# Kernel optimization log

Measured on AMD Instinct MI355X. Metric: run time of the kernel, lower is better.

## Reference

```python
import jax, jax.numpy as jnp
import numpy as np

HEADS = 8
DIM_HEAD = 64
DIM = 512
HIDDEN = HEADS * DIM_HEAD  # 512


def setup_inputs() -> dict:
    key = jax.random.key(0)
    k1, k2, k3, k4 = jax.random.split(key, 4)
    b, m, n = 4, 8, 512
    x = jax.random.normal(k1, (b, m, n, DIM), dtype=jnp.float32)
    pos_bias = jax.random.normal(k2, (HEADS, n, 16, 16), dtype=jnp.float32)
    # torch nn.Linear(dim, 3*hidden) weight is [3*hidden, dim]; we store the
    # transposed matmul form [dim, 3*hidden] for y = x @ W.
    w_qkv = jax.random.normal(k3, (DIM, 3 * HIDDEN), dtype=jnp.float32) * (DIM ** -0.5)
    w_out = jax.random.normal(k4, (HIDDEN, DIM), dtype=jnp.float32) * (HIDDEN ** -0.5)
    return {"x": x, "pos_bias": pos_bias, "w_qkv": w_qkv, "w_out": w_out}


def reference(x, pos_bias, w_qkv, w_out):
    b, m, n, _ = x.shape
    h, d = HEADS, DIM_HEAD
    scale = d ** -0.5
    qkv = jnp.einsum('bmnc,ce->bmne', x, w_qkv)  # [b,m,n,3*hidden]
    q, k, v = jnp.split(qkv, 3, axis=-1)
    # 'b m n (h d) -> (b m) h n d'
    def to_heads(t):
        return t.reshape(b * m, n, h, d).transpose(0, 2, 1, 3)
    q, k, v = to_heads(q), to_heads(k), to_heads(v)
    q = q * scale
    sim = jnp.einsum('bhid,bhjd->bhij', q, k)  # [(b*m), h, n, n]
    # pos_bias [h, n, p, q] -> mean over last two dims -> [h, n] -> broadcast [1,h,n,1]
    pb = pos_bias.mean(axis=(-2, -1))[None, :, :, None]
    sim = sim + pb
    sim = sim - jax.lax.stop_gradient(jnp.max(sim, axis=-1, keepdims=True))
    attn = jax.nn.softmax(sim, axis=-1)
    out = jnp.einsum('bhij,bhjd->bhid', attn, v)  # [(b*m), h, n, d]
    # '(b m) h n d -> b m n (h d)'
    out = out.transpose(0, 2, 1, 3).reshape(b, m, n, h * d)
    return jnp.einsum('bmne,ec->bmnc', out, w_out)
```

## Files before the change

kernel.cpp:

```cpp
#include <hip/hip_runtime.h>
#include <stdint.h>


typedef __attribute__((ext_vector_type(8))) short bf16x8;
typedef __attribute__((ext_vector_type(4))) float f32x4;
typedef __attribute__((ext_vector_type(4))) unsigned short us4;
typedef __attribute__((ext_vector_type(4))) float float4v;

__device__ __forceinline__ unsigned short f2b(float f) {
  union { float f; uint32_t u; } x; x.f = f;
  uint32_t r = x.u + 0x7fffu + ((x.u >> 16) & 1u);
  return (unsigned short)(r >> 16);
}

__device__ __forceinline__ uint32_t cvtpk(float lo, float hi) {
  uint32_t r;
  asm("v_cvt_pk_bf16_f32 %0, %1, %2" : "=v"(r) : "v"(lo), "v"(hi));
  return r;
}

__device__ __forceinline__ f32x4 mfma16(bf16x8 a, bf16x8 b, f32x4 c) {
  return __builtin_amdgcn_mfma_f32_16x16x32_bf16(a, b, c, 0, 0, 0);
}

__device__ __forceinline__ void gload_lds16(const unsigned short* g, unsigned short* l) {
  __builtin_amdgcn_global_load_lds(
      (const __attribute__((address_space(1))) unsigned int*)g,
      (__attribute__((address_space(3))) unsigned int*)l, 16, 0, 0);
}

__global__ __launch_bounds__(256) void prep_kernel(
    const float* __restrict__ x, unsigned short* __restrict__ xb,
    const float* __restrict__ wq, unsigned short* __restrict__ wqbT,
    const float* __restrict__ wo, unsigned short* __restrict__ wobT) {
  const int bid = blockIdx.x;
  if (bid < 8192) {
    size_t i = ((size_t)bid * 256 + threadIdx.x) * 4;
    float4v v = *(const float4v*)(x + i);
    us4 o;
#pragma unroll
    for (int j = 0; j < 4; ++j) o[j] = f2b(v[j]);
    *(us4*)(xb + i) = o;
    return;
  }
  __shared__ float tile[64][65];
  const float* src;
  unsigned short* dst;
  int R, C, bx, by;
  float scl = 1.0f;
  if (bid < 8192 + 192) {
    int q = bid - 8192;
    src = wq; dst = wqbT; R = 512; C = 1536; bx = q % 24; by = q / 24;
    if (bx * 64 < 512) scl = 0.125f;
  } else {
    int q = bid - 8384;
    src = wo; dst = wobT; R = 512; C = 512; bx = q % 8; by = q / 8;
  }
  const int tc0 = bx * 64, tr0 = by * 64;
#pragma unroll
  for (int k2 = 0; k2 < 16; ++k2) {
    int idx = threadIdx.x + k2 * 256;
    int r = idx >> 6, c = idx & 63;
    tile[r][c] = src[(size_t)(tr0 + r) * C + tc0 + c];
  }
  __syncthreads();
#pragma unroll
  for (int k2 = 0; k2 < 16; ++k2) {
    int idx = threadIdx.x + k2 * 256;
    int c = idx >> 6, r = idx & 63;
    dst[(size_t)(tc0 + c) * R + tr0 + r] = f2b(tile[r][c] * scl);
  }
}

__device__ __forceinline__ void gemm_core(
    const unsigned short* __restrict__ A, const unsigned short* __restrict__ Bt,
    int r0, int c0, unsigned short* As, unsigned short* Bs,
    f32x4 (&acc)[4][4]) {
  const int tid = threadIdx.x;
  const int lane = tid & 63;
  const int wave = tid >> 6;
  const int wr = (wave >> 1) * 64;
  const int wc = (wave & 1) * 64;
  const int l15 = lane & 15;
  const int g = lane >> 4;
  const int lsw = l15 & 7;

#pragma unroll
  for (int m = 0; m < 4; ++m)
#pragma unroll
    for (int n = 0; n < 4; ++n) acc[m][n] = (f32x4){0.f, 0.f, 0.f, 0.f};

  auto stage = [&](int kt, int b) {
#pragma unroll
    for (int i = 0; i < 4; ++i) {
      int chunk = tid + i * 256;
      int row = chunk >> 3;
      int csw = (chunk & 7) ^ (row & 7);
      gload_lds16(A + (size_t)(r0 + row) * 512 + kt + csw * 8,
                  As + b * 8192 + chunk * 8);
      gload_lds16(Bt + (size_t)(c0 + row) * 512 + kt + csw * 8,
                  Bs + b * 8192 + chunk * 8);
    }
  };

  stage(0, 0);
  asm volatile("s_waitcnt vmcnt(0)" ::: "memory");
  __builtin_amdgcn_s_barrier();

  int cur = 0;
#pragma unroll
  for (int t = 0; t < 8; ++t) {
    if (t < 7) stage((t + 1) * 64, cur ^ 1);
    const unsigned short* as = As + cur * 8192;
    const unsigned short* bs = Bs + cur * 8192;
#pragma unroll
    for (int ks = 0; ks < 2; ++ks) {
      bf16x8 af[4], bfr[4];
      const int cj = ((g + ks * 4) ^ lsw) * 8;
#pragma unroll
      for (int m = 0; m < 4; ++m)
        af[m] = *(const bf16x8*)(as + (wr + m * 16 + l15) * 64 + cj);
#pragma unroll
      for (int n = 0; n < 4; ++n)
        bfr[n] = *(const bf16x8*)(bs + (wc + n * 16 + l15) * 64 + cj);
      __builtin_amdgcn_s_setprio(1);
#pragma unroll
      for (int m = 0; m < 4; ++m)
#pragma unroll
        for (int n = 0; n < 4; ++n) acc[m][n] = mfma16(af[m], bfr[n], acc[m][n]);
      __builtin_amdgcn_s_setprio(0);
    }
    if (t < 7) {
      asm volatile("s_waitcnt vmcnt(0)" ::: "memory");
      __builtin_amdgcn_s_barrier();
      cur ^= 1;
    }
  }
  __syncthreads();
}

__global__ __launch_bounds__(256) void gemm_qkv_kernel(
    const unsigned short* __restrict__ xb, const unsigned short* __restrict__ wqbT,
    unsigned short* __restrict__ qb, unsigned short* __restrict__ kb,
    unsigned short* __restrict__ vtb) {
  __shared__ unsigned short smem[32768];
  f32x4 acc[4][4];
  const int bid = blockIdx.x;
  const int wgid = (bid & 7) * 192 + (bid >> 3);
  const int r0 = (wgid / 12) * 128;
  const int c0 = (wgid % 12) * 128;
  gemm_core(xb, wqbT, r0, c0, smem, smem + 16384, acc);

  const int tid = threadIdx.x, lane = tid & 63, wave = tid >> 6;
  const int wr = (wave >> 1) * 64, wc = (wave & 1) * 64;
  const int l15 = lane & 15, g = lane >> 4;
  const int part = c0 >> 9;

  if (part < 2) {
#pragma unroll
    for (int m = 0; m < 4; ++m) {
      int rbase = wr + m * 16 + 4 * g;
#pragma unroll
      for (int n = 0; n < 4; ++n) {
        int c = wc + n * 16 + l15;
        int c2 = c >> 3, ci = c & 7;
#pragma unroll
        for (int rr = 0; rr < 4; ++rr) {
          int r = rbase + rr;
          smem[r * 128 + ((c2 ^ (r & 15)) << 3) + ci] = f2b(acc[m][n][rr]);
        }
      }
    }
    __syncthreads();
    unsigned short* dstb = (part == 0) ? qb : kb;
#pragma unroll
    for (int it = 0; it < 8; ++it) {
      int idx = tid + it * 256;
      int r = idx >> 4, c2 = idx & 15;
      bf16x8 v = *(const bf16x8*)(smem + r * 128 + ((c2 ^ (r & 15)) << 3));
      int e = c0 + c2 * 8;
      int rem = e & 511, h = rem >> 6, d = rem & 63;
      int ig = r0 + r;
      int bh = (ig >> 9) * 8 + h, i = ig & 511;
      *(bf16x8*)(dstb + ((size_t)bh * 512 + i) * 64 + d) = v;
    }
  } else {
#pragma unroll
    for (int m = 0; m < 4; ++m) {
      int rbase = wr + m * 16 + 4 * g;
      int r2 = rbase >> 3, rhalf = rbase & 7;
#pragma unroll
      for (int n = 0; n < 4; ++n) {
        int c = wc + n * 16 + l15;
        us4 v;
#pragma unroll
        for (int rr = 0; rr < 4; ++rr) v[rr] = f2b(acc[m][n][rr]);
        *(us4*)(smem + c * 128 + ((r2 ^ (c & 15)) << 3) + rhalf) = v;
      }
    }
    __syncthreads();
#pragma unroll
    for (int it = 0; it < 8; ++it) {
      int idx = tid + it * 256;
      int c = idx >> 4, r8 = idx & 15;
      bf16x8 v = *(const bf16x8*)(smem + c * 128 + ((r8 ^ (c & 15)) << 3));
      int e = c0 + c;
      int rem = e & 511, h = rem >> 6, d = rem & 63;
      int ig0 = r0 + r8 * 8;
      int bh = (ig0 >> 9) * 8 + h, i = ig0 & 511;
      *(bf16x8*)(vtb + ((size_t)bh * 64 + d) * 512 + i) = v;
    }
  }
}

__global__ __launch_bounds__(256) void gemm_out_kernel(
    const unsigned short* __restrict__ ao, const unsigned short* __restrict__ wobT,
    float* __restrict__ out) {
  __shared__ unsigned short smem[32768];
  f32x4 acc[4][4];
  const int bid = blockIdx.x;
  const int wgid = (bid & 7) * 64 + (bid >> 3);
  const int r0 = (wgid >> 2) * 128;
  const int c0 = (wgid & 3) * 128;
  gemm_core(ao, wobT, r0, c0, smem, smem + 16384, acc);

  const int tid = threadIdx.x, lane = tid & 63, wave = tid >> 6;
  const int wr = (wave >> 1) * 64, wc = (wave & 1) * 64;
  const int l15 = lane & 15, g = lane >> 4;
#pragma unroll
  for (int m = 0; m < 4; ++m) {
    int i0g = r0 + wr + m * 16 + 4 * g;
#pragma unroll
    for (int n = 0; n < 4; ++n) {
      int e = c0 + wc + n * 16 + l15;
#pragma unroll
      for (int rr = 0; rr < 4; ++rr)
        out[(size_t)(i0g + rr) * 512 + e] = acc[m][n][rr];
    }
  }
}

__global__ __launch_bounds__(512, 4) void attn_kernel(
    const unsigned short* __restrict__ qb, const unsigned short* __restrict__ kb,
    const unsigned short* __restrict__ vtb, unsigned short* __restrict__ ao) {
  __shared__ unsigned short kbuf[2][8192];
  __shared__ unsigned short vbuf[2][8192];
  __shared__ unsigned short Ps[8][16][40];
  const int bh = blockIdx.x;
  const int qt = blockIdx.y;
  const int tid = threadIdx.x, lane = tid & 63, wave = tid >> 6;
  const int l15 = lane & 15, g = lane >> 4;
  const int qrow0 = qt * 128 + wave * 16;

  const unsigned short* Q = qb + ((size_t)bh * 512 + qrow0) * 64;
  const unsigned short* Kp = kb + (size_t)bh * 512 * 64;
  const unsigned short* Vt = vtb + (size_t)bh * 64 * 512;

  bf16x8 qf0 = *(const bf16x8*)(Q + l15 * 64 + g * 8);
  bf16x8 qf1 = *(const bf16x8*)(Q + l15 * 64 + 32 + g * 8);

  const int krow = tid >> 3;
  const int kck = (tid & 7) ^ (krow & 7);
  const int vrow = tid >> 4;
  const int vck = (tid & 15) ^ (vrow & 15);

  auto stage = [&](int t, int b) {
    const unsigned short* ks = Kp + ((size_t)t * 128 + krow) * 64 + kck * 8;
    gload_lds16(ks, kbuf[b] + tid * 8);
    gload_lds16(ks + 64 * 64, kbuf[b] + tid * 8 + 4096);
    const unsigned short* vs = Vt + (size_t)vrow * 512 + t * 128 + vck * 8;
    gload_lds16(vs, vbuf[b] + tid * 8);
    gload_lds16(vs + 32 * 512, vbuf[b] + tid * 8 + 4096);
  };

  f32x4 oacc[4];
#pragma unroll
  for (int m = 0; m < 4; ++m) oacc[m] = (f32x4){0.f, 0.f, 0.f, 0.f};
  float srow[4] = {0.f, 0.f, 0.f, 0.f};

  stage(0, 0);
  asm volatile("s_waitcnt vmcnt(0)" ::: "memory");
  __builtin_amdgcn_s_barrier();

  int cur = 0;
#pragma unroll
  for (int t = 0; t < 4; ++t) {
    if (t < 3) stage(t + 1, cur ^ 1);

    const unsigned short* kb_ = kbuf[cur];
    f32x4 s[8];
    const int c0i = g ^ (l15 & 7);
    __builtin_amdgcn_s_setprio(1);
#pragma unroll
    for (int tt = 0; tt < 8; ++tt) {
      int row = tt * 16 + l15;
      bf16x8 b0 = *(const bf16x8*)(kb_ + (row * 8 + c0i) * 8);
      bf16x8 b1 = *(const bf16x8*)(kb_ + (row * 8 + (c0i ^ 4)) * 8);
      f32x4 c = (f32x4){0.f, 0.f, 0.f, 0.f};
      c = mfma16(qf0, b0, c);
      s[tt] = mfma16(qf1, b1, c);
    }
    __builtin_amdgcn_s_setprio(0);

#pragma unroll
    for (int tt = 0; tt < 8; ++tt)
#pragma unroll
      for (int rr = 0; rr < 4; ++rr) {
        float e = __expf(s[tt][rr]);
        s[tt][rr] = e;
        srow[rr] += e;
      }

    const unsigned short* vb_ = vbuf[cur];
#pragma unroll
    for (int cc = 0; cc < 4; ++cc) {
#pragma unroll
      for (int rr = 0; rr < 4; ++rr) {
        uint32_t pk = cvtpk(s[cc * 2][rr], s[cc * 2 + 1][rr]);
        Ps[wave][4 * g + rr][l15] = (unsigned short)pk;
        Ps[wave][4 * g + rr][16 + l15] = (unsigned short)(pk >> 16);
      }
      asm volatile("s_waitcnt lgkmcnt(0)" ::: "memory");
      bf16x8 pf = *(const bf16x8*)(&Ps[wave][l15][g * 8]);
      __builtin_amdgcn_s_setprio(1);
#pragma unroll
      for (int m = 0; m < 4; ++m) {
        int vr = m * 16 + l15;
        bf16x8 vf = *(const bf16x8*)(vb_ + (vr * 16 + ((cc * 4 + g) ^ l15)) * 8);
        oacc[m] = mfma16(vf, pf, oacc[m]);
      }
      __builtin_amdgcn_s_setprio(0);
    }

    if (t < 3) {
      asm volatile("s_waitcnt vmcnt(0)" ::: "memory");
      __builtin_amdgcn_s_barrier();
      cur ^= 1;
    }
  }

#pragma unroll
  for (int rr = 0; rr < 4; ++rr)
#pragma unroll
    for (int o = 1; o < 16; o <<= 1) srow[rr] += __shfl_xor(srow[rr], o);
  int srcl = (l15 >> 2) * 16;
  float t0 = __shfl(srow[0], srcl), t1 = __shfl(srow[1], srcl);
  float t2 = __shfl(srow[2], srcl), t3 = __shfl(srow[3], srcl);
  int rq = l15 & 3;
  float sq = rq == 0 ? t0 : rq == 1 ? t1 : rq == 2 ? t2 : t3;
  float invq = 1.0f / sq;

  const int hh = bh & 7, bm = bh >> 3;
  unsigned short* aorow = ao + ((size_t)bm * 512 + qrow0 + l15) * 512 + hh * 64;
#pragma unroll
  for (int m = 0; m < 4; ++m) {
    union { us4 u; uint32_t w[2]; } uv;
    uv.w[0] = cvtpk(oacc[m][0] * invq, oacc[m][1] * invq);
    uv.w[1] = cvtpk(oacc[m][2] * invq, oacc[m][3] * invq);
    *(us4*)(aorow + m * 16 + 4 * g) = uv.u;
  }
}

extern "C" void kernel_launch(void* const* d_in, const int* in_sizes, int n_in,
                              void* d_out, int out_size, void* d_ws, size_t ws_size,
                              hipStream_t stream) {
  const float* x = (const float*)d_in[0];
  const float* w_qkv = (const float*)d_in[2];
  const float* w_out = (const float*)d_in[3];
  float* out = (float*)d_out;

  char* ws = (char*)d_ws;
  const size_t SZ_XB = 16384ull * 512 * 2;
  const size_t SZ_WQ = 1536ull * 512 * 2;
  const size_t SZ_WO = 512ull * 512 * 2;
  const size_t SZ_HB = 256ull * 512 * 64 * 2;
  unsigned short* xb = (unsigned short*)(ws);
  unsigned short* wqbT = (unsigned short*)(ws + SZ_XB);
  unsigned short* wobT = (unsigned short*)(ws + SZ_XB + SZ_WQ);
  unsigned short* qb = (unsigned short*)(ws + SZ_XB + SZ_WQ + SZ_WO);
  unsigned short* kb = (unsigned short*)(ws + SZ_XB + SZ_WQ + SZ_WO + SZ_HB);
  unsigned short* vtb = (unsigned short*)(ws + SZ_XB + SZ_WQ + SZ_WO + 2 * SZ_HB);
  unsigned short* ao = (unsigned short*)(ws + SZ_XB + SZ_WQ + SZ_WO + 3 * SZ_HB);

  prep_kernel<<<8448, 256, 0, stream>>>(x, xb, w_qkv, wqbT, w_out, wobT);
  gemm_qkv_kernel<<<1536, 256, 0, stream>>>(xb, wqbT, qb, kb, vtb);
  attn_kernel<<<dim3(256, 4), 512, 0, stream>>>(qb, kb, vtb, ao);
  gemm_out_kernel<<<512, 256, 0, stream>>>(ao, wobT, out);
}
```

Measured before the change: 91.02 us.

## Load full K/V per head into LDS once and loop over query tiles

The attention kernel now uses one block per (batch*m, head), loads the whole K and V^T (64KB each) into LDS in one go, and loops over the four 128-row query tiles inside the block. Before, four blocks each streamed K/V with double buffering. The aim is to cut redundant global K/V reads and the per-tile barriers. In exchange the grid shrinks from 1024 to 256 blocks, about 130KB of LDS allows roughly one block per CU, and there is no overlap between the loads and compute.

```diff
diff --git a/kernel.cpp b/kernel.cpp
--- a/kernel.cpp
+++ b/kernel.cpp
@@ -240,124 +240,114 @@
   }
 }
 
-__global__ __launch_bounds__(512, 4) void attn_kernel(
+__global__ __launch_bounds__(512, 1) void attn_kernel(
     const unsigned short* __restrict__ qb, const unsigned short* __restrict__ kb,
     const unsigned short* __restrict__ vtb, unsigned short* __restrict__ ao) {
-  __shared__ unsigned short kbuf[2][8192];
-  __shared__ unsigned short vbuf[2][8192];
+  __shared__ unsigned short Kl[32768];
+  __shared__ unsigned short Vl[32768];
   __shared__ unsigned short Ps[8][16][40];
   const int bh = blockIdx.x;
-  const int qt = blockIdx.y;
   const int tid = threadIdx.x, lane = tid & 63, wave = tid >> 6;
   const int l15 = lane & 15, g = lane >> 4;
-  const int qrow0 = qt * 128 + wave * 16;
-
-  const unsigned short* Q = qb + ((size_t)bh * 512 + qrow0) * 64;
+
   const unsigned short* Kp = kb + (size_t)bh * 512 * 64;
   const unsigned short* Vt = vtb + (size_t)bh * 64 * 512;
 
-  bf16x8 qf0 = *(const bf16x8*)(Q + l15 * 64 + g * 8);
-  bf16x8 qf1 = *(const bf16x8*)(Q + l15 * 64 + 32 + g * 8);
-
-  const int krow = tid >> 3;
-  const int kck = (tid & 7) ^ (krow & 7);
-  const int vrow = tid >> 4;
-  const int vck = (tid & 15) ^ (vrow & 15);
-
-  auto stage = [&](int t, int b) {
-    const unsigned short* ks = Kp + ((size_t)t * 128 + krow) * 64 + kck * 8;
-    gload_lds16(ks, kbuf[b] + tid * 8);
-    gload_lds16(ks + 64 * 64, kbuf[b] + tid * 8 + 4096);
-    const unsigned short* vs = Vt + (size_t)vrow * 512 + t * 128 + vck * 8;
-    gload_lds16(vs, vbuf[b] + tid * 8);
-    gload_lds16(vs + 32 * 512, vbuf[b] + tid * 8 + 4096);
-  };
-
-  f32x4 oacc[4];
-#pragma unroll
-  for (int m = 0; m < 4; ++m) oacc[m] = (f32x4){0.f, 0.f, 0.f, 0.f};
-  float srow[4] = {0.f, 0.f, 0.f, 0.f};
-
-  stage(0, 0);
+#pragma unroll
+  for (int i = 0; i < 8; ++i) {
+    int chunk = tid + i * 512;
+    int krow = chunk >> 3;
+    int kcs = (chunk & 7) ^ (krow & 7);
+    gload_lds16(Kp + (size_t)krow * 64 + kcs * 8, Kl + chunk * 8);
+    int vrow = chunk >> 6;
+    int vc = chunk & 63;
+    int vcs = (vc & 56) | ((vc & 7) ^ (vrow & 7));
+    gload_lds16(Vt + (size_t)vrow * 512 + vcs * 8, Vl + chunk * 8);
+  }
   asm volatile("s_waitcnt vmcnt(0)" ::: "memory");
   __builtin_amdgcn_s_barrier();
 
-  int cur = 0;
-#pragma unroll
-  for (int t = 0; t < 4; ++t) {
-    if (t < 3) stage(t + 1, cur ^ 1);
-
-    const unsigned short* kb_ = kbuf[cur];
-    f32x4 s[8];
-    const int c0i = g ^ (l15 & 7);
-    __builtin_amdgcn_s_setprio(1);
-#pragma unroll
-    for (int tt = 0; tt < 8; ++tt) {
-      int row = tt * 16 + l15;
-      bf16x8 b0 = *(const bf16x8*)(kb_ + (row * 8 + c0i) * 8);
-      bf16x8 b1 = *(const bf16x8*)(kb_ + (row * 8 + (c0i ^ 4)) * 8);
-      f32x4 c = (f32x4){0.f, 0.f, 0.f, 0.f};
-      c = mfma16(qf0, b0, c);
-      s[tt] = mfma16(qf1, b1, c);
-    }
-    __builtin_amdgcn_s_setprio(0);
-
-#pragma unroll
-    for (int tt = 0; tt < 8; ++tt)
-#pragma unroll
-      for (int rr = 0; rr < 4; ++rr) {
-        float e = __expf(s[tt][rr]);
-        s[tt][rr] = e;
-        srow[rr] += e;
-      }
-
-    const unsigned short* vb_ = vbuf[cur];
-#pragma unroll
-    for (int cc = 0; cc < 4; ++cc) {
-#pragma unroll
-      for (int rr = 0; rr < 4; ++rr) {
-        uint32_t pk = cvtpk(s[cc * 2][rr], s[cc * 2 + 1][rr]);
-        Ps[wave][4 * g + rr][l15] = (unsigned short)pk;
-        Ps[wave][4 * g + rr][16 + l15] = (unsigned short)(pk >> 16);
-      }
-      asm volatile("s_waitcnt lgkmcnt(0)" ::: "memory");
-      bf16x8 pf = *(const bf16x8*)(&Ps[wave][l15][g * 8]);
+  const int hh = bh & 7, bm = bh >> 3;
+  const int c0i = g ^ (l15 & 7);
+  const int vlo = l15 & 7;
+
+  for (int qt = 0; qt < 4; ++qt) {
+    const int qrow0 = qt * 128 + wave * 16;
+    const unsigned short* Q = qb + ((size_t)bh * 512 + qrow0) * 64;
+    bf16x8 qf0 = *(const bf16x8*)(Q + l15 * 64 + g * 8);
+    bf16x8 qf1 = *(const bf16x8*)(Q + l15 * 64 + 32 + g * 8);
+
+    f32x4 oacc[4];
+#pragma unroll
+    for (int m = 0; m < 4; ++m) oacc[m] = (f32x4){0.f, 0.f, 0.f, 0.f};
+    float srow[4] = {0.f, 0.f, 0.f, 0.f};
+
+#pragma unroll
+    for (int t = 0; t < 4; ++t) {
+      f32x4 s[8];
       __builtin_amdgcn_s_setprio(1);
 #pragma unroll
-      for (int m = 0; m < 4; ++m) {
-        int vr = m * 16 + l15;
-        bf16x8 vf = *(const bf16x8*)(vb_ + (vr * 16 + ((cc * 4 + g) ^ l15)) * 8);
-        oacc[m] = mfma16(vf, pf, oacc[m]);
+      for (int tt = 0; tt < 8; ++tt) {
+        int row = t * 128 + tt * 16 + l15;
+        bf16x8 b0 = *(const bf16x8*)(Kl + (row * 8 + c0i) * 8);
+        bf16x8 b1 = *(const bf16x8*)(Kl + (row * 8 + (c0i ^ 4)) * 8);
+        f32x4 c = (f32x4){0.f, 0.f, 0.f, 0.f};
+        c = mfma16(qf0, b0, c);
+        s[tt] = mfma16(qf1, b1, c);
       }
       __builtin_amdgcn_s_setprio(0);
-    }
-
-    if (t < 3) {
-      asm volatile("s_waitcnt vmcnt(0)" ::: "memory");
-      __builtin_amdgcn_s_barrier();
-      cur ^= 1;
-    }
-  }
-
-#pragma unroll
-  for (int rr = 0; rr < 4; ++rr)
-#pragma unroll
-    for (int o = 1; o < 16; o <<= 1) srow[rr] += __shfl_xor(srow[rr], o);
-  int srcl = (l15 >> 2) * 16;
-  float t0 = __shfl(srow[0], srcl), t1 = __shfl(srow[1], srcl);
-  float t2 = __shfl(srow[2], srcl), t3 = __shfl(srow[3], srcl);
-  int rq = l15 & 3;
-  float sq = rq == 0 ? t0 : rq == 1 ? t1 : rq == 2 ? t2 : t3;
-  float invq = 1.0f / sq;
-
-  const int hh = bh & 7, bm = bh >> 3;
-  unsigned short* aorow = ao + ((size_t)bm * 512 + qrow0 + l15) * 512 + hh * 64;
-#pragma unroll
-  for (int m = 0; m < 4; ++m) {
-    union { us4 u; uint32_t w[2]; } uv;
-    uv.w[0] = cvtpk(oacc[m][0] * invq, oacc[m][1] * invq);
-    uv.w[1] = cvtpk(oacc[m][2] * invq, oacc[m][3] * invq);
-    *(us4*)(aorow + m * 16 + 4 * g) = uv.u;
+
+#pragma unroll
+      for (int tt = 0; tt < 8; ++tt)
+#pragma unroll
+        for (int rr = 0; rr < 4; ++rr) {
+          float e = __expf(s[tt][rr]);
+          s[tt][rr] = e;
+          srow[rr] += e;
+        }
+
+#pragma unroll
+      for (int cc = 0; cc < 4; ++cc) {
+#pragma unroll
+        for (int rr = 0; rr < 4; ++rr) {
+          uint32_t pk = cvtpk(s[cc * 2][rr], s[cc * 2 + 1][rr]);
+          Ps[wave][4 * g + rr][l15] = (unsigned short)pk;
+          Ps[wave][4 * g + rr][16 + l15] = (unsigned short)(pk >> 16);
+        }
+        asm volatile("s_waitcnt lgkmcnt(0)" ::: "memory");
+        bf16x8 pf = *(const bf16x8*)(&Ps[wave][l15][g * 8]);
+        __builtin_amdgcn_s_setprio(1);
+#pragma unroll
+        for (int m = 0; m < 4; ++m) {
+          int vr = m * 16 + l15;
+          int ch = t * 16 + cc * 4 + g;
+          int chs = (ch & 56) | ((ch & 7) ^ vlo);
+          bf16x8 vf = *(const bf16x8*)(Vl + (vr * 64 + chs) * 8);
+          oacc[m] = mfma16(vf, pf, oacc[m]);
+        }
+        __builtin_amdgcn_s_setprio(0);
+      }
+    }
+
+#pragma unroll
+    for (int rr = 0; rr < 4; ++rr)
+#pragma unroll
+      for (int o = 1; o < 16; o <<= 1) srow[rr] += __shfl_xor(srow[rr], o);
+    int srcl = (l15 >> 2) * 16;
+    float t0 = __shfl(srow[0], srcl), t1 = __shfl(srow[1], srcl);
+    float t2 = __shfl(srow[2], srcl), t3 = __shfl(srow[3], srcl);
+    int rq = l15 & 3;
+    float sq = rq == 0 ? t0 : rq == 1 ? t1 : rq == 2 ? t2 : t3;
+    float invq = 1.0f / sq;
+
+    unsigned short* aorow = ao + ((size_t)bm * 512 + qrow0 + l15) * 512 + hh * 64;
+#pragma unroll
+    for (int m = 0; m < 4; ++m) {
+      union { us4 u; uint32_t w[2]; } uv;
+      uv.w[0] = cvtpk(oacc[m][0] * invq, oacc[m][1] * invq);
+      uv.w[1] = cvtpk(oacc[m][2] * invq, oacc[m][3] * invq);
+      *(us4*)(aorow + m * 16 + 4 * g) = uv.u;
+    }
   }
 }
 
@@ -384,6 +374,6 @@
 
   prep_kernel<<<8448, 256, 0, stream>>>(x, xb, w_qkv, wqbT, w_out, wobT);
   gemm_qkv_kernel<<<1536, 256, 0, stream>>>(xb, wqbT, qb, kb, vtb);
-  attn_kernel<<<dim3(256, 4), 512, 0, stream>>>(qb, kb, vtb, ao);
+  attn_kernel<<<256, 512, 0, stream>>>(qb, kb, vtb, ao);
   gemm_out_kernel<<<512, 256, 0, stream>>>(ao, wobT, out);
 }
```

Measured after the change: 92.41 us. No clear change (+1.5%).
